# Optimization experiments

Hardware: AMD Instinct MI355X
Metric: run time of the kernel (lower is better)

The kernel has to match this reference:

```python
import jax, jax.numpy as jnp
import numpy as np

I2 = 256   # 2 * input_size
H2 = 256   # 2 * h_size
B, N, M = 64, 1024, 1024


def setup_inputs() -> dict:
    key = jax.random.key(0)
    ks = jax.random.split(key, 12)
    s_i2 = 1.0 / np.sqrt(I2)
    s_h2 = 1.0 / np.sqrt(H2)
    s_4i = 1.0 / np.sqrt(2 * I2)
    return {
        "up": jax.random.normal(ks[0], (B, N, I2), dtype=jnp.float32),
        "uq": jax.random.normal(ks[1], (B, M, I2), dtype=jnp.float32),
        # module-internal randn tensors, made explicit for determinism
        "v0": jax.random.normal(ks[2], (B, H2), dtype=jnp.float32),
        "V": jax.random.normal(ks[3], (B, H2, 1), dtype=jnp.float32),
        # linear weights, torch Linear convention y = x @ W.T, W: [out, in]
        "Wp": jax.random.normal(ks[4], (H2, I2), dtype=jnp.float32) * s_i2,
        "Wq": jax.random.normal(ks[5], (H2, I2), dtype=jnp.float32) * s_i2,
        "Wv": jax.random.normal(ks[6], (H2, H2), dtype=jnp.float32) * s_h2,
        "Wg": jax.random.normal(ks[7], (2 * I2, 2 * I2), dtype=jnp.float32) * s_4i,
        # GRUCell params: gates ordered (r, z, n)
        "w_ih": jax.random.normal(ks[8], (3 * H2, I2), dtype=jnp.float32) * s_h2,
        "w_hh": jax.random.normal(ks[9], (3 * H2, H2), dtype=jnp.float32) * s_h2,
        "b_ih": jax.random.normal(ks[10], (3 * H2,), dtype=jnp.float32) * s_h2,
        "b_hh": jax.random.normal(ks[11], (3 * H2,), dtype=jnp.float32) * s_h2,
    }


def _gru_cell(x, h, w_ih, w_hh, b_ih, b_hh):
    gi = x @ w_ih.T + b_ih          # [b, 3H]
    gh = h @ w_hh.T + b_hh          # [b, 3H]
    i_r, i_z, i_n = jnp.split(gi, 3, axis=1)
    h_r, h_z, h_n = jnp.split(gh, 3, axis=1)
    r = jax.nn.sigmoid(i_r + h_r)
    z = jax.nn.sigmoid(i_z + h_z)
    n = jnp.tanh(i_n + r * h_n)
    return (1.0 - z) * n + z * h


def reference(up, uq, v0, V, Wp, Wq, Wv, Wg, w_ih, w_hh, b_ih, b_hh):
    # up: [b, n, 2i], uq: [b, m, 2i]
    Up = jnp.transpose(up, (1, 0, 2))       # [n, b, 2i]
    Uq = jnp.transpose(uq, (1, 0, 2))       # [m, b, 2i]
    Uq_ = uq                                 # [b, m, 2i]
    Wuq = Uq @ Wq.T                          # [m, b, 2h] (loop-invariant)
    Vv = V[:, :, 0]                          # [b, 2h]

    def step(v, up_i):
        x = jnp.tanh(up_i @ Wp.T + Wuq + v @ Wv.T)       # [m, b, 2h]
        s = jnp.einsum('mbh,bh->bm', x, Vv)               # attention scores
        a = jax.nn.softmax(s, axis=1)                     # [b, m]
        c = jnp.einsum('bm,bmi->bi', a, Uq_)              # [b, 2i]
        r = jnp.concatenate([up_i, c], axis=1)            # [b, 4i]
        g = jax.nn.sigmoid(r @ Wg.T)
        c_ = (g * r)[:, I2:]                              # gated context [b, 2i]
        v_new = _gru_cell(c_, v, w_ih, w_hh, b_ih, b_hh)
        return v_new, v_new

    _, vs = jax.lax.scan(step, v0, Up)       # vs: [n, b, 2h]
    return vs  # dropout with p=0 is identity
```

## Files before the change

### kernel.cpp

```cpp
#include <hip/hip_runtime.h>

#define Bn 64
#define Nn 1024
#define Mn 1024
#define GSTR 16384
#define KSCALE 2.8853900817779268f

typedef unsigned short u16;
typedef _Float16 h2 __attribute__((ext_vector_type(2)));

__device__ __forceinline__ float us2f(u16 u) {
    _Float16 h = __builtin_bit_cast(_Float16, u);
    return (float)h;
}
__device__ __forceinline__ u16 f2h(float f) {
    _Float16 h = (_Float16)f;
    return __builtin_bit_cast(u16, h);
}
__device__ __forceinline__ float rcp_fast(float x) {
#if __has_builtin(__builtin_amdgcn_rcpf)
    return __builtin_amdgcn_rcpf(x);
#else
    return 1.0f / x;
#endif
}
__device__ __forceinline__ float exp2_fast(float x) {
#if __has_builtin(__builtin_amdgcn_exp2f)
    return __builtin_amdgcn_exp2f(x);
#else
    return exp2f(x);
#endif
}
__device__ __forceinline__ float wsum(float x) {
#pragma unroll
    for (int m = 32; m > 0; m >>= 1) x += __shfl_xor(x, m, 64);
    return x;
}
__device__ __forceinline__ float wmax(float x) {
#pragma unroll
    for (int m = 32; m > 0; m >>= 1) x = fmaxf(x, __shfl_xor(x, m, 64));
    return x;
}
__device__ __forceinline__ float dot2(unsigned a, unsigned b, float c) {
#if __has_builtin(__builtin_amdgcn_fdot2)
    return __builtin_amdgcn_fdot2(__builtin_bit_cast(h2, a), __builtin_bit_cast(h2, b), c, false);
#else
    h2 av = __builtin_bit_cast(h2, a), bv = __builtin_bit_cast(h2, b);
    return c + (float)av.x * (float)bv.x + (float)av.y * (float)bv.y;
#endif
}
__device__ __forceinline__ void agst(float* p, float v) {
    __hip_atomic_store(p, v, __ATOMIC_RELAXED, __HIP_MEMORY_SCOPE_AGENT);
}
__device__ __forceinline__ float agld(float* p) {
    return __hip_atomic_load(p, __ATOMIC_RELAXED, __HIP_MEMORY_SCOPE_AGENT);
}
__device__ __forceinline__ void agstu(unsigned* p, unsigned v) {
    __hip_atomic_store(p, v, __ATOMIC_RELAXED, __HIP_MEMORY_SCOPE_AGENT);
}
__device__ __forceinline__ unsigned agldu(unsigned* p) {
    return __hip_atomic_load(p, __ATOMIC_RELAXED, __HIP_MEMORY_SCOPE_AGENT);
}

__global__ __launch_bounds__(256)
void gemm_f16(const float* __restrict__ U, const float* __restrict__ W,
              u16* __restrict__ outN, u16* __restrict__ outT,
              int transposed, float scale) {
    __shared__ float WL[256 * 33];
    __shared__ float uL[32 * 33];
    const int tid = threadIdx.x;
    const size_t row0 = (size_t)blockIdx.x * 32;
    float acc[32];
#pragma unroll
    for (int m = 0; m < 32; ++m) acc[m] = 0.f;
    for (int ic = 0; ic < 8; ++ic) {
        __syncthreads();
        for (int e = tid; e < 8192; e += 256) {
            int h = e >> 5, ii = e & 31;
            WL[h * 33 + ii] = W[h * 256 + ic * 32 + ii];
        }
        for (int e = tid; e < 1024; e += 256) {
            int r = e >> 5, ii = e & 31;
            uL[r * 33 + ii] = U[(row0 + r) * 256 + ic * 32 + ii];
        }
        __syncthreads();
#pragma unroll 4
        for (int ii = 0; ii < 32; ++ii) {
            float w = WL[tid * 33 + ii];
#pragma unroll
            for (int m = 0; m < 32; ++m)
                acc[m] = fmaf(w, uL[m * 33 + ii], acc[m]);
        }
    }
    if (!transposed) {
#pragma unroll
        for (int m = 0; m < 32; ++m)
            outN[(row0 + m) * 256 + tid] = f2h(scale * acc[m]);
    } else {
        __syncthreads();
#pragma unroll
        for (int m = 0; m < 32; ++m) WL[tid * 33 + m] = acc[m];
        __syncthreads();
        const size_t batch = row0 >> 10;
        const int m0 = (int)(row0 & 1023);
        for (int e = tid; e < 8192; e += 256) {
            int h = e >> 5, mm = e & 31;
            outT[(batch * 256 + h) * 1024 + m0 + mm] = f2h(scale * WL[h * 33 + mm]);
        }
    }
}

__global__ void pack8(const float* __restrict__ src, u16* __restrict__ dst,
                      int R, int C, float scale) {
    int idx = blockIdx.x * blockDim.x + threadIdx.x;
    int total = R * (C >> 3);
    if (idx >= total) return;
    int c8 = idx / R, r = idx - c8 * R;
    u16 pk[8];
#pragma unroll
    for (int e = 0; e < 8; ++e) pk[e] = f2h(scale * src[(size_t)r * C + c8 * 8 + e]);
    *(uint4*)&dst[(size_t)idx * 8] = *(uint4*)pk;
}

__global__ __launch_bounds__(256)
void uq_pack(const float* __restrict__ uq, u16* __restrict__ out) {
    __shared__ float T[32][65];
    const int blk = blockIdx.x;
    const int ib = blk & 3, mt = (blk >> 2) & 31, b = blk >> 7;
    const int tid = threadIdx.x;
#pragma unroll
    for (int s = 0; s < 8; ++s) {
        int idx = tid + 256 * s, mm = idx >> 6, ii = idx & 63;
        T[mm][ii] = uq[((size_t)b * 1024 + mt * 32 + mm) * 256 + ib * 64 + ii];
    }
    __syncthreads();
    const int mo = tid >> 6, ii = tid & 63;
    u16 pk[8];
#pragma unroll
    for (int e = 0; e < 8; ++e) pk[e] = f2h(T[mo * 8 + e][ii]);
    *(uint4*)&out[(((size_t)b * 128 + mt * 4 + mo) * 256 + ib * 64 + ii) * 8] = *(uint4*)pk;
}

__global__ __launch_bounds__(1024, 4)
void scan_kernel(const float* __restrict__ up, const float* __restrict__ v0,
                 const float* __restrict__ V, const float* __restrict__ b_ih,
                 const float* __restrict__ b_hh,
                 const u16* __restrict__ WuqT, const u16* __restrict__ Pm,
                 const u16* __restrict__ uqP, const u16* __restrict__ WvP,
                 const u16* __restrict__ wihP, const u16* __restrict__ whhP,
                 const u16* __restrict__ Wg2P,
                 float* __restrict__ out, unsigned int* __restrict__ ctrs,
                 float* __restrict__ gdata) {
    const int tid = threadIdx.x;
    const int bid = blockIdx.x;
    const int x = bid & 7, q = (bid >> 3) & 3, bhi = bid >> 5;
    const int b = (bhi << 3) | x;

    unsigned int* flag0 = ctrs + b * 16;
    unsigned int* flag1 = ctrs + b * 16 + 4;
    float* gb = gdata + (size_t)b * GSTR;
    float* cpartF = gb;
    float* mlsB   = gb + 1024;
    unsigned* gpkB = (unsigned*)(gb + 1032);

    __shared__ __align__(16) u16 WuqL[256 * 256];
    __shared__ __align__(16) float scratch[2048];
    __shared__ __align__(16) float giL[768], ghL[768];
    __shared__ __align__(16) float2 dvLds[256];
    __shared__ __align__(16) float vLds[256], pnLds[256];
    __shared__ __align__(16) u16 eH[256], rH[512], vHu[256], cH[64];
    __shared__ __align__(16) float bihs[768], bhhs[768];
    __shared__ float red[32];
    __shared__ float svv_sh;

    {
        const unsigned* src32 = (const unsigned*)(WuqT + (size_t)b * 256 * 1024);
        unsigned* dst32 = (unsigned*)WuqL;
        for (int d = tid; d < 32768; d += 1024) {
            int h = d >> 7, mp = d & 127;
            dst32[d] = src32[h * 512 + q * 128 + mp];
        }
    }
    if (tid < 768) { bihs[tid] = b_ih[tid]; bhhs[tid] = b_hh[tid]; }
    float vvreg = 0.f;
    if (tid < 256) {
        float v = v0[b * 256 + tid];
        vLds[tid] = v;
        vHu[tid] = f2h(v);
        vvreg = 2.0f * V[b * 256 + tid];
        pnLds[tid] = us2f(Pm[(size_t)b * Nn * 256 + tid]);
    }
    __syncthreads();
    {
        float s = wsum(vvreg);
        if ((tid & 63) == 0) red[tid >> 6] = s;
    }
    {
        const int h = tid & 255, jc = tid >> 8;
        const uint4* wv = (const uint4*)WvP;
        const unsigned* vH32 = (const unsigned*)vHu;
        float acc = 0.f;
#pragma unroll
        for (int l = 0; l < 8; ++l) {
            uint4 Wd = wv[(size_t)(jc * 8 + l) * 256 + h];
            int vb = jc * 32 + l * 4;
            acc = dot2(Wd.x, vH32[vb + 0], acc);
            acc = dot2(Wd.y, vH32[vb + 1], acc);
            acc = dot2(Wd.z, vH32[vb + 2], acc);
            acc = dot2(Wd.w, vH32[vb + 3], acc);
        }
        scratch[jc * 256 + h] = acc;
    }
    __syncthreads();
    if (tid == 0) svv_sh = 0.5f * (red[0] + red[1] + red[2] + red[3]);
    if (tid < 256)
        dvLds[tid] = make_float2(pnLds[tid] + scratch[tid] + scratch[256 + tid] +
                                 scratch[512 + tid] + scratch[768 + tid], vvreg);
    __syncthreads();
    const float SVv = svv_sh;

    const float* up_b = up + (size_t)b * Nn * 256;

    const int iD = tid & 255, mcD = tid >> 8;
    uint4 U0, U1, U2, U3, U4, U5, U6, U7;
    {
        const uint4* uqrow = (const uint4*)(uqP + (size_t)b * 128 * 256 * 8) +
                             (size_t)(q * 32 + mcD * 8) * 256 + iD;
        U0 = uqrow[0 * 256]; U1 = uqrow[1 * 256];
        U2 = uqrow[2 * 256]; U3 = uqrow[3 * 256];
        U4 = uqrow[4 * 256]; U5 = uqrow[5 * 256];
        U6 = uqrow[6 * 256]; U7 = uqrow[7 * 256];
    }

    long long budget = 1LL << 26;
    float mloc, sumloc;

    for (int t = 0; t < Nn; ++t) {
        const unsigned tgt = (unsigned)(t + 1);
        asm volatile("" : "+v"(U0.x), "+v"(U0.y), "+v"(U0.z), "+v"(U0.w),
                          "+v"(U1.x), "+v"(U1.y), "+v"(U1.z), "+v"(U1.w),
                          "+v"(U2.x), "+v"(U2.y), "+v"(U2.z), "+v"(U2.w),
                          "+v"(U3.x), "+v"(U3.y), "+v"(U3.z), "+v"(U3.w));
        asm volatile("" : "+v"(U4.x), "+v"(U4.y), "+v"(U4.z), "+v"(U4.w),
                          "+v"(U5.x), "+v"(U5.y), "+v"(U5.z), "+v"(U5.w),
                          "+v"(U6.x), "+v"(U6.y), "+v"(U6.z), "+v"(U6.w),
                          "+v"(U7.x), "+v"(U7.y), "+v"(U7.z), "+v"(U7.w));
        float upv = 0.f;
        if (tid < 256)
            upv = __builtin_nontemporal_load(&up_b[(size_t)t * 256 + tid]);

        {
            const int m2 = (tid & 127) * 2;
            const int hc = tid >> 7;
            float a0 = 0.f, a1 = 0.f;
            const u16* wrow = &WuqL[(hc * 32) * 256 + m2];
#pragma unroll 8
            for (int hh = 0; hh < 32; ++hh) {
                float2 dv = dvLds[hc * 32 + hh];
                unsigned w2 = *(const unsigned*)wrow;
                wrow += 256;
                float w0 = us2f((u16)(w2 & 0xffffu));
                float w1 = us2f((u16)(w2 >> 16));
                a0 = fmaf(dv.y, rcp_fast(1.f + exp2_fast(w0 + dv.x)), a0);
                a1 = fmaf(dv.y, rcp_fast(1.f + exp2_fast(w1 + dv.x)), a1);
            }
            ((float2*)scratch)[hc * 128 + (tid & 127)] = make_float2(a0, a1);
        }
        __syncthreads();

        {
            const int m = tid & 255;
            float sv = SVv;
#pragma unroll
            for (int c2 = 0; c2 < 8; ++c2) sv -= scratch[c2 * 256 + m];
            if (tid >= 256) sv = -3.0e38f;
            float mx = wmax(sv);
            if ((tid & 63) == 0) red[tid >> 6] = mx;
            __syncthreads();
            mloc = red[0];
#pragma unroll
            for (int w2 = 1; w2 < 16; ++w2) mloc = fmaxf(mloc, red[w2]);
            float ev = __expf(sv - mloc);
            if (tid < 256) eH[m] = f2h(ev);
            float sm = wsum(ev);
            if ((tid & 63) == 0) red[16 + (tid >> 6)] = sm;
            __syncthreads();
            sumloc = red[16] + red[17] + red[18] + red[19];
        }

        {
            const unsigned* eH32 = (const unsigned*)eH;
            float acc = 0.f;
            int eb = mcD * 32;
            acc = dot2(U0.x, eH32[eb + 0], acc);  acc = dot2(U0.y, eH32[eb + 1], acc);
            acc = dot2(U0.z, eH32[eb + 2], acc);  acc = dot2(U0.w, eH32[eb + 3], acc);
            acc = dot2(U1.x, eH32[eb + 4], acc);  acc = dot2(U1.y, eH32[eb + 5], acc);
            acc = dot2(U1.z, eH32[eb + 6], acc);  acc = dot2(U1.w, eH32[eb + 7], acc);
            acc = dot2(U2.x, eH32[eb + 8], acc);  acc = dot2(U2.y, eH32[eb + 9], acc);
            acc = dot2(U2.z, eH32[eb + 10], acc); acc = dot2(U2.w, eH32[eb + 11], acc);
            acc = dot2(U3.x, eH32[eb + 12], acc); acc = dot2(U3.y, eH32[eb + 13], acc);
            acc = dot2(U3.z, eH32[eb + 14], acc); acc = dot2(U3.w, eH32[eb + 15], acc);
            acc = dot2(U4.x, eH32[eb + 16], acc); acc = dot2(U4.y, eH32[eb + 17], acc);
            acc = dot2(U4.z, eH32[eb + 18], acc); acc = dot2(U4.w, eH32[eb + 19], acc);
            acc = dot2(U5.x, eH32[eb + 20], acc); acc = dot2(U5.y, eH32[eb + 21], acc);
            acc = dot2(U5.z, eH32[eb + 22], acc); acc = dot2(U5.w, eH32[eb + 23], acc);
            acc = dot2(U6.x, eH32[eb + 24], acc); acc = dot2(U6.y, eH32[eb + 25], acc);
            acc = dot2(U6.z, eH32[eb + 26], acc); acc = dot2(U6.w, eH32[eb + 27], acc);
            acc = dot2(U7.x, eH32[eb + 28], acc); acc = dot2(U7.y, eH32[eb + 29], acc);
            acc = dot2(U7.z, eH32[eb + 30], acc); acc = dot2(U7.w, eH32[eb + 31], acc);
            scratch[mcD * 256 + iD] = acc;
        }
        __syncthreads();
        if (tid < 256)
            agst(&cpartF[q * 256 + tid], scratch[tid] + scratch[256 + tid] +
                                         scratch[512 + tid] + scratch[768 + tid]);
        if (tid == 0) { agst(&mlsB[2 * q], mloc); agst(&mlsB[2 * q + 1], sumloc); }
        __syncthreads();

        if (tid == 0) {
            asm volatile("s_waitcnt vmcnt(0)" ::: "memory");
            agstu(&flag0[q], tgt);
        }
        float ghv = 0.f;
        if (tid < 768) {
            const uint4* wh = (const uint4*)whhP;
            const unsigned* vH32 = (const unsigned*)vHu;
#pragma unroll
            for (int l = 0; l < 8; ++l) {
                uint4 Hd = wh[(size_t)(q * 8 + l) * 768 + tid];
                int vb = q * 32 + l * 4;
                ghv = dot2(Hd.x, vH32[vb + 0], ghv);
                ghv = dot2(Hd.y, vH32[vb + 1], ghv);
                ghv = dot2(Hd.z, vH32[vb + 2], ghv);
                ghv = dot2(Hd.w, vH32[vb + 3], ghv);
            }
            ghL[tid] = ghv;
        }
        if (tid < 4) {
            while (agldu(&flag0[tid]) < tgt) {
                __builtin_amdgcn_s_sleep(1);
                if (--budget < 0) break;
            }
        }
        __syncthreads();

        {
            if (tid < 256) {
                float cp0 = agld(&cpartF[tid]);       float cp1 = agld(&cpartF[256 + tid]);
                float cp2 = agld(&cpartF[512 + tid]); float cp3 = agld(&cpartF[768 + tid]);
                float m0 = agld(&mlsB[0]), s0 = agld(&mlsB[1]);
                float m1 = agld(&mlsB[2]), s1 = agld(&mlsB[3]);
                float m2 = agld(&mlsB[4]), s2 = agld(&mlsB[5]);
                float m3 = agld(&mlsB[6]), s3 = agld(&mlsB[7]);
                float Mg = fmaxf(fmaxf(m0, m1), fmaxf(m2, m3));
                float w0 = __expf(m0 - Mg), w1 = __expf(m1 - Mg);
                float w2 = __expf(m2 - Mg), w3 = __expf(m3 - Mg);
                float denom = s0 * w0 + s1 * w1 + s2 * w2 + s3 * w3;
                float c = cp0 * w0 + cp1 * w1 + cp2 * w2 + cp3 * w3;
                c *= rcp_fast(denom);
                rH[tid] = f2h(upv);
                rH[256 + tid] = f2h(c);
            }
            __syncthreads();
        }

        {
            const int o = tid & 63, ks = tid >> 6;
            const uint4* wg = (const uint4*)Wg2P;
            const unsigned* rH32 = (const unsigned*)rH;
            float acc = 0.f;
#pragma unroll
            for (int l = 0; l < 4; ++l) {
                int k8 = ks * 4 + l;
                uint4 Wd = wg[(size_t)k8 * 256 + q * 64 + o];
                int kb = k8 * 4;
                acc = dot2(Wd.x, rH32[kb + 0], acc);
                acc = dot2(Wd.y, rH32[kb + 1], acc);
                acc = dot2(Wd.z, rH32[kb + 2], acc);
                acc = dot2(Wd.w, rH32[kb + 3], acc);
            }
            scratch[ks * 64 + o] = acc;
        }
        __syncthreads();
        if (tid < 64) {
            float acc = 0.f;
#pragma unroll
            for (int c2 = 0; c2 < 16; ++c2) acc += scratch[c2 * 64 + tid];
            float g = rcp_fast(1.f + __expf(-acc));
            cH[tid] = f2h(g * us2f(rH[256 + 64 * q + tid]));
        }
        __syncthreads();

        if (tid < 768) {
            const uint4* wi = (const uint4*)wihP;
            const unsigned* cH32 = (const unsigned*)cH;
            float gi = 0.f;
#pragma unroll
            for (int l = 0; l < 8; ++l) {
                uint4 Wd = wi[(size_t)(q * 8 + l) * 768 + tid];
                int kb = l * 4;
                gi = dot2(Wd.x, cH32[kb + 0], gi);
                gi = dot2(Wd.y, cH32[kb + 1], gi);
                gi = dot2(Wd.z, cH32[kb + 2], gi);
                gi = dot2(Wd.w, cH32[kb + 3], gi);
            }
            unsigned pk = (unsigned)f2h(gi) | ((unsigned)f2h(ghv) << 16);
            agstu(&gpkB[q * 768 + tid], pk);
            giL[tid] = gi;
        } else if (t + 1 < Nn) {
            const int h = tid - 768;
            pnLds[h] = us2f(Pm[((size_t)b * Nn + t + 1) * 256 + h]);
        }
        __syncthreads();

        if (tid == 0) {
            asm volatile("s_waitcnt vmcnt(0)" ::: "memory");
            agstu(&flag1[q], tgt);
        }
        if (tid < 4) {
            while (agldu(&flag1[tid]) < tgt) {
                __builtin_amdgcn_s_sleep(1);
                if (--budget < 0) break;
            }
        }
        __syncthreads();

        if (tid < 256) {
            const int h = tid;
            float gir = bihs[h] + giL[h], giz = bihs[256 + h] + giL[256 + h];
            float gin = bihs[512 + h] + giL[512 + h];
            float ghr = bhhs[h] + ghL[h], ghz = bhhs[256 + h] + ghL[256 + h];
            float ghn = bhhs[512 + h] + ghL[512 + h];
#pragma unroll
            for (int s = 0; s < 4; ++s) {
                if (s == q) continue;
                unsigned* gp = &gpkB[s * 768];
                unsigned p0 = agldu(&gp[h]);
                unsigned p1 = agldu(&gp[256 + h]);
                unsigned p2 = agldu(&gp[512 + h]);
                gir += us2f((u16)(p0 & 0xffffu)); ghr += us2f((u16)(p0 >> 16));
                giz += us2f((u16)(p1 & 0xffffu)); ghz += us2f((u16)(p1 >> 16));
                gin += us2f((u16)(p2 & 0xffffu)); ghn += us2f((u16)(p2 >> 16));
            }
            float rr = rcp_fast(1.f + __expf(-(gir + ghr)));
            float zz = rcp_fast(1.f + __expf(-(giz + ghz)));
            float narg = gin + rr * ghn;
            float nn = 1.f - 2.f * rcp_fast(1.f + __expf(2.f * narg));
            float vnew = (1.f - zz) * nn + zz * vLds[h];
            if ((h >> 6) == q)
                __builtin_nontemporal_store(vnew, &out[((size_t)t * Bn + b) * 256 + h]);
            vLds[h] = vnew;
            vHu[h] = f2h(vnew);
        }
        __syncthreads();

        if (t + 1 < Nn) {
            {
                const int h = tid & 255, jc = tid >> 8;
                const uint4* wv = (const uint4*)WvP;
                const unsigned* vH32 = (const unsigned*)vHu;
                float acc = 0.f;
#pragma unroll
                for (int l = 0; l < 8; ++l) {
                    uint4 Wd = wv[(size_t)(jc * 8 + l) * 256 + h];
                    int vb = jc * 32 + l * 4;
                    acc = dot2(Wd.x, vH32[vb + 0], acc);
                    acc = dot2(Wd.y, vH32[vb + 1], acc);
                    acc = dot2(Wd.z, vH32[vb + 2], acc);
                    acc = dot2(Wd.w, vH32[vb + 3], acc);
                }
                scratch[jc * 256 + h] = acc;
            }
            __syncthreads();
            if (tid < 256)
                dvLds[tid] = make_float2(pnLds[tid] + scratch[tid] + scratch[256 + tid] +
                                         scratch[512 + tid] + scratch[768 + tid], vvreg);
            __syncthreads();
        }
    }
}

extern "C" void kernel_launch(void* const* d_in, const int* in_sizes, int n_in,
                              void* d_out, int out_size, void* d_ws, size_t ws_size,
                              hipStream_t stream) {
    const float* up   = (const float*)d_in[0];
    const float* uq   = (const float*)d_in[1];
    const float* v0   = (const float*)d_in[2];
    const float* V    = (const float*)d_in[3];
    const float* Wp   = (const float*)d_in[4];
    const float* Wq   = (const float*)d_in[5];
    const float* Wv   = (const float*)d_in[6];
    const float* Wg   = (const float*)d_in[7];
    const float* w_ih = (const float*)d_in[8];
    const float* w_hh = (const float*)d_in[9];
    const float* b_ih = (const float*)d_in[10];
    const float* b_hh = (const float*)d_in[11];
    float* out = (float*)d_out;

    char* ws = (char*)d_ws;
    unsigned int* ctrs = (unsigned int*)ws;
    float* gdata = (float*)(ws + 8192);
    u16* WuqT = (u16*)(ws + (size_t)(8u << 20));
    u16* Pm   = WuqT + (size_t)Bn * 256 * 1024;
    u16* uqP  = Pm + (size_t)Bn * Nn * 256;
    u16* WvP  = uqP + (size_t)Bn * 128 * 256 * 8;
    u16* wihP = WvP + 65536;
    u16* whhP = wihP + 196608;
    u16* Wg2P = whhP + 196608;

    hipMemsetAsync(ctrs, 0, 4096, stream);

    hipLaunchKernelGGL(gemm_f16, dim3(2048), dim3(256), 0, stream,
                       uq, Wq, (u16*)nullptr, WuqT, 1, KSCALE);
    hipLaunchKernelGGL(gemm_f16, dim3(2048), dim3(256), 0, stream,
                       up, Wp, Pm, (u16*)nullptr, 0, KSCALE);
    hipLaunchKernelGGL(uq_pack, dim3(8192), dim3(256), 0, stream, uq, uqP);
    hipLaunchKernelGGL(pack8, dim3(32), dim3(256), 0, stream, Wv, WvP, 256, 256, KSCALE);
    hipLaunchKernelGGL(pack8, dim3(96), dim3(256), 0, stream, w_ih, wihP, 768, 256, 1.0f);
    hipLaunchKernelGGL(pack8, dim3(96), dim3(256), 0, stream, w_hh, whhP, 768, 256, 1.0f);
    hipLaunchKernelGGL(pack8, dim3(64), dim3(256), 0, stream, Wg + 512 * 256, Wg2P, 256, 512, 1.0f);

    hipLaunchKernelGGL(scan_kernel, dim3(256), dim3(1024), 0, stream,
                       up, v0, V, b_ih, b_hh,
                       WuqT, Pm, uqP, WvP, wihP, whhP, Wg2P,
                       out, ctrs, gdata);
}
```

Baseline: 20.33 ms.

## Use per-wave local softmax max and overlap up-half Wg GEMV with flag wait

The softmax inside each block now subtracts a per-wavefront max instead of a block-wide max, and rescales the four wave partials afterwards. This removes two __syncthreads and a cross-wave max reduction per step. The half of the Wg gate matvec that depends only on the up_i input is moved before the inter-block flag spin-wait, so it overlaps with waiting for the other blocks. The cost is extra exp evaluations for the rescaling and some reordering of which threads run which work, which could shift register pressure.

```diff
diff --git a/kernel.cpp b/kernel.cpp
--- a/kernel.cpp
+++ b/kernel.cpp
@@ -233,7 +233,6 @@
     }
 
     long long budget = 1LL << 26;
-    float mloc, sumloc;
 
     for (int t = 0; t < Nn; ++t) {
         const unsigned tgt = (unsigned)(t + 1);
@@ -268,25 +267,18 @@
         }
         __syncthreads();
 
-        {
-            const int m = tid & 255;
+        if (tid < 256) {
+            const int m = tid;
             float sv = SVv;
 #pragma unroll
             for (int c2 = 0; c2 < 8; ++c2) sv -= scratch[c2 * 256 + m];
-            if (tid >= 256) sv = -3.0e38f;
             float mx = wmax(sv);
-            if ((tid & 63) == 0) red[tid >> 6] = mx;
-            __syncthreads();
-            mloc = red[0];
-#pragma unroll
-            for (int w2 = 1; w2 < 16; ++w2) mloc = fmaxf(mloc, red[w2]);
-            float ev = __expf(sv - mloc);
-            if (tid < 256) eH[m] = f2h(ev);
+            float ev = __expf(sv - mx);
+            eH[m] = f2h(ev);
             float sm = wsum(ev);
-            if ((tid & 63) == 0) red[16 + (tid >> 6)] = sm;
-            __syncthreads();
-            sumloc = red[16] + red[17] + red[18] + red[19];
-        }
+            if ((tid & 63) == 0) { red[tid >> 6] = mx; red[16 + (tid >> 6)] = sm; }
+        }
+        __syncthreads();
 
         {
             const unsigned* eH32 = (const unsigned*)eH;
@@ -311,10 +303,22 @@
             scratch[mcD * 256 + iD] = acc;
         }
         __syncthreads();
-        if (tid < 256)
-            agst(&cpartF[q * 256 + tid], scratch[tid] + scratch[256 + tid] +
-                                         scratch[512 + tid] + scratch[768 + tid]);
-        if (tid == 0) { agst(&mlsB[2 * q], mloc); agst(&mlsB[2 * q + 1], sumloc); }
+
+        if (tid < 256) {
+            float m0 = red[0], m1 = red[1], m2 = red[2], m3 = red[3];
+            float mloc = fmaxf(fmaxf(m0, m1), fmaxf(m2, m3));
+            float s0 = __expf(m0 - mloc), s1 = __expf(m1 - mloc);
+            float s2 = __expf(m2 - mloc), s3 = __expf(m3 - mloc);
+            float cp = scratch[tid] * s0 + scratch[256 + tid] * s1 +
+                       scratch[512 + tid] * s2 + scratch[768 + tid] * s3;
+            agst(&cpartF[q * 256 + tid], cp);
+            rH[tid] = f2h(upv);
+            if (tid == 0) {
+                float sumloc = red[16] * s0 + red[17] * s1 + red[18] * s2 + red[19] * s3;
+                agst(&mlsB[2 * q], mloc);
+                agst(&mlsB[2 * q + 1], sumloc);
+            }
+        }
         __syncthreads();
 
         if (tid == 0) {
@@ -335,6 +339,23 @@
                 ghv = dot2(Hd.w, vH32[vb + 3], ghv);
             }
             ghL[tid] = ghv;
+        }
+        if (tid < 512) {
+            const int o = tid & 63, ks = tid >> 6;
+            const uint4* wg = (const uint4*)Wg2P;
+            const unsigned* rH32 = (const unsigned*)rH;
+            float acc = 0.f;
+#pragma unroll
+            for (int l = 0; l < 4; ++l) {
+                int k8 = ks * 4 + l;
+                uint4 Wd = wg[(size_t)k8 * 256 + q * 64 + o];
+                int kb = k8 * 4;
+                acc = dot2(Wd.x, rH32[kb + 0], acc);
+                acc = dot2(Wd.y, rH32[kb + 1], acc);
+                acc = dot2(Wd.z, rH32[kb + 2], acc);
+                acc = dot2(Wd.w, rH32[kb + 3], acc);
+            }
+            scratch[ks * 64 + o] = acc;
         }
         if (tid < 4) {
             while (agldu(&flag0[tid]) < tgt) {
@@ -358,13 +379,12 @@
                 float denom = s0 * w0 + s1 * w1 + s2 * w2 + s3 * w3;
                 float c = cp0 * w0 + cp1 * w1 + cp2 * w2 + cp3 * w3;
                 c *= rcp_fast(denom);
-                rH[tid] = f2h(upv);
                 rH[256 + tid] = f2h(c);
             }
             __syncthreads();
         }
 
-        {
+        if (tid >= 512) {
             const int o = tid & 63, ks = tid >> 6;
             const uint4* wg = (const uint4*)Wg2P;
             const unsigned* rH32 = (const unsigned*)rH;
```

After: 23.12 ms. +13.7%, slower.
